# Performance work log

Measured on AMD Instinct MI355X. Metric: run time of the kernel, lower is better.

Reference implementation:

```python
import jax, jax.numpy as jnp
import numpy as np

T, HW, C = 64, 24, 1024
MID = 256
WIN = 2  # 'video' forward_type -> 2x2 windows


def setup_inputs() -> dict:
    key = jax.random.key(0)
    k1, k2, k3, k4, k5 = jax.random.split(key, 5)
    return {
        "image_features": jax.random.normal(k1, (T, HW * HW, C), dtype=jnp.float32),
        "Wq": jax.random.normal(k2, (C, MID), dtype=jnp.float32) * 0.02,
        "bq": jax.random.normal(k3, (MID,), dtype=jnp.float32) * 0.02,
        "Wk": jax.random.normal(k4, (C, MID), dtype=jnp.float32) * 0.02,
        "bk": jax.random.normal(k5, (MID,), dtype=jnp.float32) * 0.02,
    }


def reference(image_features, Wq, bq, Wk, bk):
    # forward_type == 'video': 2x2 windowed attention over pooled patches
    t, n, c = image_features.shape
    H = W = int(np.sqrt(n))
    h2, w2 = H // WIN, W // WIN
    # [T, H, W, C] -> [T, h2, 2, w2, 2, C] -> [T, h2, w2, 2, 2, C] -> [T, P, 4, C]
    x = image_features.reshape(t, h2, WIN, w2, WIN, c)
    windows = x.transpose(0, 1, 3, 2, 4, 5).reshape(t, h2 * w2, WIN * WIN, c)
    # avg_pool2d(2,2) == mean over each 2x2 window
    pooled = windows.mean(axis=2)  # [T, P, C]
    q = pooled @ Wq + bq           # [T, P, MID]
    k = windows @ Wk + bk          # [T, P, 4, MID]
    scale = 1.0 / jnp.sqrt(jnp.float32(MID))
    attn = jnp.einsum("tpd,tpwd->tpw", q, k) * scale  # [T, P, 4]
    attn = jnp.nan_to_num(attn)
    attn = jax.nn.softmax(attn, axis=-1)
    attn_feat = jnp.einsum("tpw,tpwc->tpc", attn, windows)  # softmax-weighted value avg
    # query dim has size 1, so .mean(1) in torch is identity here
    return pooled + attn_feat  # [T, P, C]; new_image_size = (h2, w2) is static
```

## Files before the change

### kernel.cpp

```cpp
#include <hip/hip_runtime.h>

#define T_ 64
#define P_ 144
#define NPAIR 9216
#define C_ 1024
#define MID_ 256

typedef __attribute__((ext_vector_type(4))) float f32x4;
typedef __attribute__((ext_vector_type(8))) __bf16 bf16x8;
typedef __attribute__((ext_vector_type(4))) __bf16 bf16x4;

__device__ __forceinline__ void async_copy16(const void* g, void* l) {
  __builtin_amdgcn_global_load_lds(
      (const __attribute__((address_space(1))) unsigned int*)g,
      (__attribute__((address_space(3))) unsigned int*)l, 16, 0, 0);
}

__global__ void prep_kernel(const float* __restrict__ img,
                            const float* __restrict__ Wq,
                            const float* __restrict__ bq,
                            const float* __restrict__ Wk,
                            __bf16* __restrict__ poolb,
                            __bf16* __restrict__ Wqb,
                            __bf16* __restrict__ Wkb,
                            float* __restrict__ kb) {
  const int bid = blockIdx.x;
  const int tid = threadIdx.x;
  if (bid < NPAIR) {
    const int t = bid / P_;
    const int p = bid - t * P_;
    const int wy = p / 12, wx = p - wy * 12;
    const int c = tid * 4;
    const float* base = img + ((size_t)t * 576 + 48 * wy + 2 * wx) * C_;
    f32x4 s = *(const f32x4*)(base + c);
    s += *(const f32x4*)(base + (size_t)1 * C_ + c);
    s += *(const f32x4*)(base + (size_t)24 * C_ + c);
    s += *(const f32x4*)(base + (size_t)25 * C_ + c);
    s *= 0.25f;
    bf16x4 pv;
#pragma unroll
    for (int j = 0; j < 4; ++j) pv[j] = (__bf16)s[j];
    *(bf16x4*)(poolb + (size_t)bid * C_ + c) = pv;
  } else if (bid < NPAIR + 256) {
    const int c0 = (bid - NPAIR) * 1024 + tid * 4;
    f32x4 q = *(const f32x4*)(Wq + c0);
    f32x4 k = *(const f32x4*)(Wk + c0);
    bf16x4 qb, kbv;
#pragma unroll
    for (int j = 0; j < 4; ++j) { qb[j] = (__bf16)q[j]; kbv[j] = (__bf16)k[j]; }
    *(bf16x4*)(Wqb + c0) = qb;
    *(bf16x4*)(Wkb + c0) = kbv;
  } else {
    __shared__ float bqs[256];
    bqs[tid] = bq[tid];
    __syncthreads();
    const int n = (bid - (NPAIR + 256)) * 256 + tid;
    const float* row = Wk + (size_t)n * MID_;
    float s = 0.f;
#pragma unroll 4
    for (int j = 0; j < 256; ++j) s += row[j] * bqs[j];
    kb[n] = s;
  }
}

template <typename OutT, bool HasBias>
__global__ __launch_bounds__(256) void gemm_kernel(
    const __bf16* __restrict__ A, const __bf16* __restrict__ Bt,
    const float* __restrict__ bias, OutT* __restrict__ C,
    int K, int ntiles, int ldc) {
  __shared__ __align__(16) __bf16 As[128 * 32];
  __shared__ __align__(16) __bf16 Bs[128 * 32];
  const int bid = blockIdx.x;
  const int mt = bid / ntiles, nt = bid - mt * ntiles;
  const int tid = threadIdx.x;
  const int lane = tid & 63;
  const int wv = tid >> 6;
  const int quad = lane >> 4, lr = lane & 15;
  const int wm = wv >> 1, wn = wv & 1;

  const int r0 = tid >> 2, p0 = tid & 3;
  const int wvb = (tid & ~63) * 16;
  const __bf16* ga0 = A + ((size_t)mt * 128 + r0) * (size_t)K + p0 * 8;
  const __bf16* ga1 = ga0 + (size_t)64 * K;
  const __bf16* gb0 = Bt + ((size_t)nt * 128 + r0) * (size_t)K + p0 * 8;
  const __bf16* gb1 = gb0 + (size_t)64 * K;
  char* AsB0 = (char*)As + wvb;
  char* AsB1 = (char*)As + 4096 + wvb;
  char* BsB0 = (char*)Bs + wvb;
  char* BsB1 = (char*)Bs + 4096 + wvb;

  f32x4 acc[4][4] = {};
  const int iters = K >> 5;

  for (int it = 0; it < iters; ++it) {
    async_copy16(ga0, AsB0);
    async_copy16(ga1, AsB1);
    async_copy16(gb0, BsB0);
    async_copy16(gb1, BsB1);
    ga0 += 32; ga1 += 32; gb0 += 32; gb1 += 32;
    __syncthreads();

    bf16x8 a[4], b[4];
    const bf16x8* Ap = (const bf16x8*)As;
    const bf16x8* Bp = (const bf16x8*)Bs;
#pragma unroll
    for (int i = 0; i < 4; ++i) {
      a[i] = Ap[(wm * 64 + i * 16 + lr) * 4 + quad];
      b[i] = Bp[(wn * 64 + i * 16 + lr) * 4 + quad];
    }
#pragma unroll
    for (int mi = 0; mi < 4; ++mi)
#pragma unroll
      for (int ni = 0; ni < 4; ++ni)
        acc[mi][ni] = __builtin_amdgcn_mfma_f32_16x16x32_bf16(
            a[mi], b[ni], acc[mi][ni], 0, 0, 0);
    __syncthreads();
  }

  const int colb = nt * 128 + wn * 64;
  const int rowb = mt * 128 + wm * 64 + quad * 4;
#pragma unroll
  for (int ni = 0; ni < 4; ++ni) {
    const int col = colb + ni * 16 + lr;
    const float bv = HasBias ? bias[col] : 0.f;
#pragma unroll
    for (int mi = 0; mi < 4; ++mi) {
      const int row = rowb + mi * 16;
#pragma unroll
      for (int r = 0; r < 4; ++r)
        C[(size_t)(row + r) * ldc + col] = (OutT)(acc[mi][ni][r] + bv);
    }
  }
}

__global__ void attn_out_kernel(const float* __restrict__ U,
                                const float* __restrict__ img,
                                float* __restrict__ out) {
  const int pair = blockIdx.x;
  const int tid = threadIdx.x;
  const int wv = tid >> 6, lane = tid & 63;
  __shared__ float red[4][4];

  const int t = pair / P_;
  const int pp = pair - t * P_;
  const int wy = pp / 12, wx = pp - wy * 12;
  const float* base = img + ((size_t)t * 576 + 48 * wy + 2 * wx) * C_;
  const int c = tid * 4;
  f32x4 v0 = *(const f32x4*)(base + c);
  f32x4 v1 = *(const f32x4*)(base + (size_t)1 * C_ + c);
  f32x4 v2 = *(const f32x4*)(base + (size_t)24 * C_ + c);
  f32x4 v3 = *(const f32x4*)(base + (size_t)25 * C_ + c);
  const f32x4 u4 = *(const f32x4*)(U + (size_t)pair * C_ + c);

  float pd[4];
#pragma unroll
  for (int j = 0; j < 4; ++j) {
  }
  pd[0] = u4[0] * v0[0] + u4[1] * v0[1] + u4[2] * v0[2] + u4[3] * v0[3];
  pd[1] = u4[0] * v1[0] + u4[1] * v1[1] + u4[2] * v1[2] + u4[3] * v1[3];
  pd[2] = u4[0] * v2[0] + u4[1] * v2[1] + u4[2] * v2[2] + u4[3] * v2[3];
  pd[3] = u4[0] * v3[0] + u4[1] * v3[1] + u4[2] * v3[2] + u4[3] * v3[3];

#pragma unroll
  for (int w = 0; w < 4; ++w) {
    float p = pd[w];
    p += __shfl_down(p, 32);
    p += __shfl_down(p, 16);
    p += __shfl_down(p, 8);
    p += __shfl_down(p, 4);
    p += __shfl_down(p, 2);
    p += __shfl_down(p, 1);
    if (lane == 0) red[w][wv] = p;
  }
  __syncthreads();
  float lg[4];
  float mx = -1e30f;
#pragma unroll
  for (int w = 0; w < 4; ++w) {
    lg[w] = (red[w][0] + red[w][1] + red[w][2] + red[w][3]) * 0.0625f;
    mx = fmaxf(mx, lg[w]);
  }
  float att[4];
  float ssum = 0.f;
#pragma unroll
  for (int w = 0; w < 4; ++w) {
    att[w] = __expf(lg[w] - mx);
    ssum += att[w];
  }
  const float inv = 1.f / ssum;
  const float a0 = att[0] * inv, a1 = att[1] * inv;
  const float a2 = att[2] * inv, a3 = att[3] * inv;

  f32x4 o = (v0 + v1 + v2 + v3) * 0.25f;
  o += a0 * v0 + a1 * v1 + a2 * v2 + a3 * v3;
  *(f32x4*)(out + (size_t)pair * C_ + c) = o;
}

extern "C" void kernel_launch(void* const* d_in, const int* in_sizes, int n_in,
                              void* d_out, int out_size, void* d_ws,
                              size_t ws_size, hipStream_t stream) {
  const float* img = (const float*)d_in[0];
  const float* Wq = (const float*)d_in[1];
  const float* bq = (const float*)d_in[2];
  const float* Wk = (const float*)d_in[3];
  const float* bk = (const float*)d_in[4];
  (void)bk;
  float* out = (float*)d_out;

  char* ws = (char*)d_ws;
  __bf16* poolb = (__bf16*)ws;
  __bf16* Wqb = (__bf16*)(ws + 18874368);
  __bf16* Wkb = (__bf16*)(ws + 19398656);
  __bf16* H = (__bf16*)(ws + 19922944);
  float* kb = (float*)(ws + 22020096);
  float* U = (float*)(ws + 22024192);

  prep_kernel<<<NPAIR + 260, 256, 0, stream>>>(img, Wq, bq, Wk, poolb, Wqb,
                                               Wkb, kb);
  gemm_kernel<__bf16, false><<<64, 256, 0, stream>>>(Wkb, Wqb, nullptr, H,
                                                     MID_, 8, C_);
  gemm_kernel<float, true><<<576, 256, 0, stream>>>(poolb, H, kb, U, C_, 8,
                                                    C_);
  attn_out_kernel<<<NPAIR, 256, 0, stream>>>(U, img, out);
}
```

Baseline: 309.0 us.

## Fuse weight conversion and Wk·Wqᵀ GEMM into prep kernel; store U as bf16

The small H = Wk·Wqᵀ GEMM now runs inside the prep kernel: 64 extra blocks load the fp32 weights, convert them to bf16 in registers and stage them in LDS. This removes the separate weight-conversion pass, its bf16 weight buffers and one kernel launch. The U GEMM output is also stored as bf16 instead of fp32, halving its write and read traffic, at the cost of some precision in the attention logits. The prep kernel now declares LDS tiles for every block, which may reduce occupancy for the pooling blocks.

```diff
diff --git a/kernel.cpp b/kernel.cpp
--- a/kernel.cpp
+++ b/kernel.cpp
@@ -16,14 +16,32 @@
       (__attribute__((address_space(3))) unsigned int*)l, 16, 0, 0);
 }
 
-__global__ void prep_kernel(const float* __restrict__ img,
-                            const float* __restrict__ Wq,
-                            const float* __restrict__ bq,
-                            const float* __restrict__ Wk,
-                            __bf16* __restrict__ poolb,
-                            __bf16* __restrict__ Wqb,
-                            __bf16* __restrict__ Wkb,
-                            float* __restrict__ kb) {
+__device__ __forceinline__ void mfma_tile(const __bf16* As, const __bf16* Bs,
+                                          int wm, int wn, int quad, int lr,
+                                          f32x4 acc[4][4]) {
+  bf16x8 a[4], b[4];
+  const bf16x8* Ap = (const bf16x8*)As;
+  const bf16x8* Bp = (const bf16x8*)Bs;
+#pragma unroll
+  for (int i = 0; i < 4; ++i) {
+    a[i] = Ap[(wm * 64 + i * 16 + lr) * 4 + quad];
+    b[i] = Bp[(wn * 64 + i * 16 + lr) * 4 + quad];
+  }
+#pragma unroll
+  for (int mi = 0; mi < 4; ++mi)
+#pragma unroll
+    for (int ni = 0; ni < 4; ++ni)
+      acc[mi][ni] = __builtin_amdgcn_mfma_f32_16x16x32_bf16(
+          a[mi], b[ni], acc[mi][ni], 0, 0, 0);
+}
+
+__global__ __launch_bounds__(256) void prep_kernel(
+    const float* __restrict__ img, const float* __restrict__ Wq,
+    const float* __restrict__ bq, const float* __restrict__ Wk,
+    __bf16* __restrict__ poolb, __bf16* __restrict__ H,
+    float* __restrict__ kb) {
+  __shared__ __align__(16) __bf16 As[128 * 32];
+  __shared__ __align__(16) __bf16 Bs[128 * 32];
   const int bid = blockIdx.x;
   const int tid = threadIdx.x;
   if (bid < NPAIR) {
@@ -41,20 +59,59 @@
 #pragma unroll
     for (int j = 0; j < 4; ++j) pv[j] = (__bf16)s[j];
     *(bf16x4*)(poolb + (size_t)bid * C_ + c) = pv;
-  } else if (bid < NPAIR + 256) {
-    const int c0 = (bid - NPAIR) * 1024 + tid * 4;
-    f32x4 q = *(const f32x4*)(Wq + c0);
-    f32x4 k = *(const f32x4*)(Wk + c0);
-    bf16x4 qb, kbv;
-#pragma unroll
-    for (int j = 0; j < 4; ++j) { qb[j] = (__bf16)q[j]; kbv[j] = (__bf16)k[j]; }
-    *(bf16x4*)(Wqb + c0) = qb;
-    *(bf16x4*)(Wkb + c0) = kbv;
+  } else if (bid < NPAIR + 64) {
+    const int b = bid - NPAIR;
+    const int mt = b >> 3, nt = b & 7;
+    const int lane = tid & 63;
+    const int wv = tid >> 6;
+    const int quad = lane >> 4, lr = lane & 15;
+    const int wm = wv >> 1, wn = wv & 1;
+    const int r0 = tid >> 2, p0 = tid & 3;
+    const float* ga0 = Wk + (size_t)(mt * 128 + r0) * MID_ + p0 * 8;
+    const float* ga1 = ga0 + (size_t)64 * MID_;
+    const float* gb0 = Wq + (size_t)(nt * 128 + r0) * MID_ + p0 * 8;
+    const float* gb1 = gb0 + (size_t)64 * MID_;
+    f32x4 acc[4][4] = {};
+    for (int it = 0; it < 8; ++it) {
+      const f32x4 a0 = *(const f32x4*)ga0, a1 = *(const f32x4*)(ga0 + 4);
+      const f32x4 a2 = *(const f32x4*)ga1, a3 = *(const f32x4*)(ga1 + 4);
+      const f32x4 b0 = *(const f32x4*)gb0, b1 = *(const f32x4*)(gb0 + 4);
+      const f32x4 b2 = *(const f32x4*)gb1, b3 = *(const f32x4*)(gb1 + 4);
+      ga0 += 32; ga1 += 32; gb0 += 32; gb1 += 32;
+      bf16x8 ca0, ca1, cb0, cb1;
+#pragma unroll
+      for (int j = 0; j < 4; ++j) {
+        ca0[j] = (__bf16)a0[j]; ca0[4 + j] = (__bf16)a1[j];
+        ca1[j] = (__bf16)a2[j]; ca1[4 + j] = (__bf16)a3[j];
+        cb0[j] = (__bf16)b0[j]; cb0[4 + j] = (__bf16)b1[j];
+        cb1[j] = (__bf16)b2[j]; cb1[4 + j] = (__bf16)b3[j];
+      }
+      *(bf16x8*)(As + (size_t)tid * 8) = ca0;
+      *(bf16x8*)(As + (size_t)(tid + 256) * 8) = ca1;
+      *(bf16x8*)(Bs + (size_t)tid * 8) = cb0;
+      *(bf16x8*)(Bs + (size_t)(tid + 256) * 8) = cb1;
+      __syncthreads();
+      mfma_tile(As, Bs, wm, wn, quad, lr, acc);
+      __syncthreads();
+    }
+    const int colb = nt * 128 + wn * 64;
+    const int rowb = mt * 128 + wm * 64 + quad * 4;
+#pragma unroll
+    for (int ni = 0; ni < 4; ++ni) {
+      const int col = colb + ni * 16 + lr;
+#pragma unroll
+      for (int mi = 0; mi < 4; ++mi) {
+        const int row = rowb + mi * 16;
+#pragma unroll
+        for (int r = 0; r < 4; ++r)
+          H[(size_t)(row + r) * C_ + col] = (__bf16)acc[mi][ni][r];
+      }
+    }
   } else {
     __shared__ float bqs[256];
     bqs[tid] = bq[tid];
     __syncthreads();
-    const int n = (bid - (NPAIR + 256)) * 256 + tid;
+    const int n = (bid - (NPAIR + 64)) * 256 + tid;
     const float* row = Wk + (size_t)n * MID_;
     float s = 0.f;
 #pragma unroll 4
@@ -63,15 +120,13 @@
   }
 }
 
-template <typename OutT, bool HasBias>
-__global__ __launch_bounds__(256) void gemm_kernel(
+__global__ __launch_bounds__(256) void gemm_u_kernel(
     const __bf16* __restrict__ A, const __bf16* __restrict__ Bt,
-    const float* __restrict__ bias, OutT* __restrict__ C,
-    int K, int ntiles, int ldc) {
+    const float* __restrict__ bias, __bf16* __restrict__ C) {
   __shared__ __align__(16) __bf16 As[128 * 32];
   __shared__ __align__(16) __bf16 Bs[128 * 32];
   const int bid = blockIdx.x;
-  const int mt = bid / ntiles, nt = bid - mt * ntiles;
+  const int mt = bid >> 3, nt = bid & 7;
   const int tid = threadIdx.x;
   const int lane = tid & 63;
   const int wv = tid >> 6;
@@ -80,40 +135,25 @@
 
   const int r0 = tid >> 2, p0 = tid & 3;
   const int wvb = (tid & ~63) * 16;
-  const __bf16* ga0 = A + ((size_t)mt * 128 + r0) * (size_t)K + p0 * 8;
-  const __bf16* ga1 = ga0 + (size_t)64 * K;
-  const __bf16* gb0 = Bt + ((size_t)nt * 128 + r0) * (size_t)K + p0 * 8;
-  const __bf16* gb1 = gb0 + (size_t)64 * K;
+  const __bf16* ga0 = A + ((size_t)mt * 128 + r0) * (size_t)C_ + p0 * 8;
+  const __bf16* ga1 = ga0 + (size_t)64 * C_;
+  const __bf16* gb0 = Bt + ((size_t)nt * 128 + r0) * (size_t)C_ + p0 * 8;
+  const __bf16* gb1 = gb0 + (size_t)64 * C_;
   char* AsB0 = (char*)As + wvb;
   char* AsB1 = (char*)As + 4096 + wvb;
   char* BsB0 = (char*)Bs + wvb;
   char* BsB1 = (char*)Bs + 4096 + wvb;
 
   f32x4 acc[4][4] = {};
-  const int iters = K >> 5;
-
-  for (int it = 0; it < iters; ++it) {
+
+  for (int it = 0; it < 32; ++it) {
     async_copy16(ga0, AsB0);
     async_copy16(ga1, AsB1);
     async_copy16(gb0, BsB0);
     async_copy16(gb1, BsB1);
     ga0 += 32; ga1 += 32; gb0 += 32; gb1 += 32;
     __syncthreads();
-
-    bf16x8 a[4], b[4];
-    const bf16x8* Ap = (const bf16x8*)As;
-    const bf16x8* Bp = (const bf16x8*)Bs;
-#pragma unroll
-    for (int i = 0; i < 4; ++i) {
-      a[i] = Ap[(wm * 64 + i * 16 + lr) * 4 + quad];
-      b[i] = Bp[(wn * 64 + i * 16 + lr) * 4 + quad];
-    }
-#pragma unroll
-    for (int mi = 0; mi < 4; ++mi)
-#pragma unroll
-      for (int ni = 0; ni < 4; ++ni)
-        acc[mi][ni] = __builtin_amdgcn_mfma_f32_16x16x32_bf16(
-            a[mi], b[ni], acc[mi][ni], 0, 0, 0);
+    mfma_tile(As, Bs, wm, wn, quad, lr, acc);
     __syncthreads();
   }
 
@@ -122,18 +162,18 @@
 #pragma unroll
   for (int ni = 0; ni < 4; ++ni) {
     const int col = colb + ni * 16 + lr;
-    const float bv = HasBias ? bias[col] : 0.f;
+    const float bv = bias[col];
 #pragma unroll
     for (int mi = 0; mi < 4; ++mi) {
       const int row = rowb + mi * 16;
 #pragma unroll
       for (int r = 0; r < 4; ++r)
-        C[(size_t)(row + r) * ldc + col] = (OutT)(acc[mi][ni][r] + bv);
+        C[(size_t)(row + r) * C_ + col] = (__bf16)(acc[mi][ni][r] + bv);
     }
   }
 }
 
-__global__ void attn_out_kernel(const float* __restrict__ U,
+__global__ void attn_out_kernel(const __bf16* __restrict__ U,
                                 const float* __restrict__ img,
                                 float* __restrict__ out) {
   const int pair = blockIdx.x;
@@ -150,12 +190,12 @@
   f32x4 v1 = *(const f32x4*)(base + (size_t)1 * C_ + c);
   f32x4 v2 = *(const f32x4*)(base + (size_t)24 * C_ + c);
   f32x4 v3 = *(const f32x4*)(base + (size_t)25 * C_ + c);
-  const f32x4 u4 = *(const f32x4*)(U + (size_t)pair * C_ + c);
+  const bf16x4 ub = *(const bf16x4*)(U + (size_t)pair * C_ + c);
+  f32x4 u4;
+#pragma unroll
+  for (int j = 0; j < 4; ++j) u4[j] = (float)ub[j];
 
   float pd[4];
-#pragma unroll
-  for (int j = 0; j < 4; ++j) {
-  }
   pd[0] = u4[0] * v0[0] + u4[1] * v0[1] + u4[2] * v0[2] + u4[3] * v0[3];
   pd[1] = u4[0] * v1[0] + u4[1] * v1[1] + u4[2] * v1[2] + u4[3] * v1[3];
   pd[2] = u4[0] * v2[0] + u4[1] * v2[1] + u4[2] * v2[2] + u4[3] * v2[3];
@@ -209,17 +249,11 @@
 
   char* ws = (char*)d_ws;
   __bf16* poolb = (__bf16*)ws;
-  __bf16* Wqb = (__bf16*)(ws + 18874368);
-  __bf16* Wkb = (__bf16*)(ws + 19398656);
-  __bf16* H = (__bf16*)(ws + 19922944);
-  float* kb = (float*)(ws + 22020096);
-  float* U = (float*)(ws + 22024192);
-
-  prep_kernel<<<NPAIR + 260, 256, 0, stream>>>(img, Wq, bq, Wk, poolb, Wqb,
-                                               Wkb, kb);
-  gemm_kernel<__bf16, false><<<64, 256, 0, stream>>>(Wkb, Wqb, nullptr, H,
-                                                     MID_, 8, C_);
-  gemm_kernel<float, true><<<576, 256, 0, stream>>>(poolb, H, kb, U, C_, 8,
-                                                    C_);
+  __bf16* H = (__bf16*)(ws + 18874368);
+  float* kb = (float*)(ws + 20971520);
+  __bf16* U = (__bf16*)(ws + 20975616);
+
+  prep_kernel<<<NPAIR + 68, 256, 0, stream>>>(img, Wq, bq, Wk, poolb, H, kb);
+  gemm_u_kernel<<<576, 256, 0, stream>>>(poolb, H, kb, U);
   attn_out_kernel<<<NPAIR, 256, 0, stream>>>(U, img, out);
 }
```

New measurement: 295.0 us. 4.5% less time.
